# Kernel optimization log

Hardware: AMD Instinct MI355X
Metric: run time of the kernel (lower is better)

## Reference

```python
import jax, jax.numpy as jnp
import numpy as np
from jax import lax

B = 512
ITER = 3  # routing iterations


def squash(x):
    # matches torch: sn/(1+sn) * x / (sqrt(sn)+1e-6), norm over last dim
    sn = jnp.sum(x * x, axis=-1, keepdims=True)
    return sn / (1.0 + sn) * x / (jnp.sqrt(sn) + 1e-6)


def conv2d(x, w, b, stride):
    y = lax.conv_general_dilated(
        x, w, window_strides=(stride, stride), padding='VALID',
        dimension_numbers=('NCHW', 'OIHW', 'NCHW'))
    return y + b[None, :, None, None]


def setup_inputs() -> dict:
    key = jax.random.key(0)
    ks = jax.random.split(key, 6)
    x = jax.random.normal(ks[0], (B, 3, 28, 28), dtype=jnp.float32)
    conv1_w = jax.random.normal(ks[1], (256, 3, 9, 9), dtype=jnp.float32) * 0.05
    conv1_b = jnp.zeros((256,), dtype=jnp.float32)
    conv2_w = jax.random.normal(ks[2], (256, 256, 9, 9), dtype=jnp.float32) * 0.02
    conv2_b = jnp.zeros((256,), dtype=jnp.float32)
    # DigitCapsule W: (1, 32, 6, 6, 10, 8, 16) in torch; drop leading 1 here
    W = jax.random.normal(ks[3], (32, 6, 6, 10, 8, 16), dtype=jnp.float32)
    return {'x': x, 'conv1_w': conv1_w, 'conv1_b': conv1_b,
            'conv2_w': conv2_w, 'conv2_b': conv2_b, 'W': W}


def reference(x, conv1_w, conv1_b, conv2_w, conv2_b, W):
    # conv1 + relu: [B,3,28,28] -> [B,256,20,20]
    h = jax.nn.relu(conv2d(x, conv1_w, conv1_b, stride=1))
    # primary capsule conv: -> [B,256,6,6]
    h = conv2d(h, conv2_w, conv2_b, stride=2)
    # torch .view(-1, 32, 6, 6, 8) on contiguous NCHW == row-major reshape
    u = squash(jnp.reshape(h, (h.shape[0], 32, 6, 6, 8)))  # [B,32,6,6,8]
    # u_hat[b,i,j,k,o,e] = sum_d u[b,i,j,k,d] * W[i,j,k,o,d,e]
    u_hat = jnp.einsum('bijkd,ijkode->bijkoe', u, W)  # [B,32,6,6,10,16]
    b_logits = jnp.zeros(u_hat.shape[:-1], dtype=u_hat.dtype)  # [B,32,6,6,10]
    v = None
    for it in range(ITER):
        c = jax.nn.softmax(b_logits, axis=-1)
        s = jnp.sum(c[..., None] * u_hat, axis=(1, 2, 3))  # [B,10,16]
        v = squash(s)
        if it < ITER - 1:
            b_logits = b_logits + jnp.sum(
                u_hat * v[:, None, None, None], axis=-1)
    return v
```

## Files before the change

### kernel.cpp

```cpp
#include <hip/hip_runtime.h>
#include <math.h>

typedef short short8v __attribute__((ext_vector_type(8)));
typedef float float4v __attribute__((ext_vector_type(4)));

#define OFF_U     ((size_t)0)
#define OFF_A     ((size_t)18874368)
#define OFF_W1T   ((size_t)29491200)
#define OFF_WT    ((size_t)30670848)
#define OFF_SPART ((size_t)33619968)
#define OFF_VSUM  ((size_t)38862848)

__device__ inline short f2bf(float f) {
  union { float f; unsigned u; } v; v.f = f;
  unsigned r = v.u + 0x7FFFu + ((v.u >> 16) & 1u);
  return (short)(r >> 16);
}
__device__ inline float bf2f(short s) {
  union { unsigned u; float f; } v; v.u = ((unsigned)(unsigned short)s) << 16;
  return v.f;
}

__global__ __launch_bounds__(256) void prep_kernel(
    const float* __restrict__ w2, short* __restrict__ w2b,
    const float* __restrict__ w1, short* __restrict__ w1t,
    const float* __restrict__ W, short* __restrict__ Wtb) {
  __shared__ short tl[81][66];
  int bx = blockIdx.x, t = threadIdx.x;
  if (bx < 1024) {
    int co = bx >> 2, ci0 = (bx & 3) * 64;
    for (int f = t; f < 64 * 81; f += 256) {
      int cip = f / 81, tap = f % 81;
      tl[tap][cip] = f2bf(w2[((size_t)co * 256 + ci0 + cip) * 81 + tap]);
    }
    __syncthreads();
    for (int f = t; f < 81 * 64; f += 256) {
      int tap = f >> 6, cip = f & 63;
      w2b[((size_t)tap * 256 + co) * 256 + ci0 + cip] = tl[tap][cip];
    }
  } else if (bx < 1280) {
    int co = bx - 1024;
    w1t[co * 256 + t] = (t < 243) ? f2bf(w1[(size_t)co * 243 + t]) : (short)0;
  } else {
    int idx = (bx - 1280) * 256 + t;
    if (idx < 1152 * 1280) {
      int n = idx / 1280, r = idx - n * 1280;
      int o = r >> 7, de = r & 127;
      int d = de >> 4, e = de & 15;
      Wtb[(((size_t)n * 10 + o) * 16 + e) * 8 + d] = f2bf(W[idx]);
    }
  }
}

__global__ __launch_bounds__(256, 2) void conv_fused_kernel(
    const float* __restrict__ x, const short* __restrict__ w1t,
    const float* __restrict__ b1v, const short* __restrict__ w2b,
    const float* __restrict__ b2v, float* __restrict__ h2) {
  __shared__ short xsb[4704];
  __shared__ short h1l[800][40];

  int b0 = blockIdx.x * 2;
  int coh = blockIdx.y;
  int t = threadIdx.x;
  int lane = t & 63;
  int wv = t >> 6;
  int l15 = lane & 15, lq = lane >> 4;

  for (int i = t; i < 4704; i += 256) xsb[i] = f2bf(x[(size_t)b0 * 2352 + i]);

  float4v acc2[5][2];
#pragma unroll
  for (int mt = 0; mt < 5; mt++)
#pragma unroll
    for (int nt = 0; nt < 2; nt++) acc2[mt][nt] = (float4v){0.f, 0.f, 0.f, 0.f};

  int rowb[5];
#pragma unroll
  for (int mt = 0; mt < 5; mt++) {
    int m = mt * 16 + l15;
    int ab = (m >= 40) ? 1 : 0;
    int s = m - 40 * ab;
    if (s >= 36) s = 0;
    int sx = (s * 43) >> 8;
    int sy = s - 6 * sx;
    rowb[mt] = ab * 400 + sx * 40 + sy * 2;
  }
  int co[2];
#pragma unroll
  for (int nt = 0; nt < 2; nt++) co[nt] = coh * 128 + wv * 32 + nt * 16 + l15;

  int nmt = (wv == 0) ? 7 : 6;
  int px1[7], py1[7];
#pragma unroll
  for (int j = 0; j < 7; j++) {
    int pos = (wv + 4 * j) * 16 + l15;
    if (pos >= 400) pos = 0;
    px1[j] = (pos * 3277) >> 16;
    py1[j] = pos - 20 * px1[j];
  }

  for (int ch = 0; ch < 8; ch++) {
    int ci0 = ch * 32;
    __syncthreads();

    for (int bb = 0; bb < 2; bb++) {
      const short* xb = &xsb[bb * 2352];
      float4v acc1[7][2];
#pragma unroll
      for (int j = 0; j < 7; j++)
#pragma unroll
        for (int nt = 0; nt < 2; nt++) acc1[j][nt] = (float4v){0.f, 0.f, 0.f, 0.f};
#pragma unroll 1
      for (int kk = 0; kk < 8; kk++) {
        int k0 = kk * 32 + lq * 8;
        int cin = (k0 * 810) >> 16;
        int rem = k0 - 81 * cin;
        int kx = (rem * 57) >> 9;
        int ky = rem - 9 * kx;
        int nv = 243 - k0; if (nv > 8) nv = 8; if (nv < 0) nv = 0;
        int n1 = 9 - ky; if (n1 > 8) n1 = 8;
        int d2 = (kx < 8) ? (28 - ky) : (560 - ky);
        short8v b1f[2];
#pragma unroll
        for (int nt = 0; nt < 2; nt++)
          b1f[nt] = *(const short8v*)(w1t + (size_t)(ci0 + nt * 16 + l15) * 256 + k0);
#pragma unroll
        for (int j = 0; j < 7; j++) {
          if (j < nmt) {
            int o1 = cin * 784 + (px1[j] + kx) * 28 + py1[j] + ky;
            short8v a;
#pragma unroll
            for (int jj = 0; jj < 8; jj++) {
              int idx = (jj < n1) ? (o1 + jj) : (o1 + d2 + jj - n1);
              if (jj >= nv) idx = 0;
              short vsh = xb[idx];
              a[jj] = (jj < nv) ? vsh : (short)0;
            }
#pragma unroll
            for (int nt = 0; nt < 2; nt++)
              acc1[j][nt] = __builtin_amdgcn_mfma_f32_16x16x32_bf16(
                  a, b1f[nt], acc1[j][nt], 0, 0, 0);
          }
        }
      }
      float bs[2];
#pragma unroll
      for (int nt = 0; nt < 2; nt++) bs[nt] = b1v[ci0 + nt * 16 + l15];
#pragma unroll
      for (int j = 0; j < 7; j++) {
        if (j < nmt) {
#pragma unroll
          for (int nt = 0; nt < 2; nt++) {
#pragma unroll
            for (int r = 0; r < 4; r++) {
              int pos = (wv + 4 * j) * 16 + lq * 4 + r;
              float h = acc1[j][nt][r] + bs[nt];
              h1l[bb * 400 + pos][nt * 16 + l15] = f2bf(h > 0.f ? h : 0.f);
            }
          }
        }
      }
    }
    __syncthreads();

    short8v bA[2], bB[2], bC[2];
#pragma unroll
    for (int nt = 0; nt < 2; nt++) {
      const short* wb = w2b + (size_t)co[nt] * 256 + ci0 + lq * 8;
      bA[nt] = *(const short8v*)(wb);
      bB[nt] = *(const short8v*)(wb + 65536);
      bC[nt] = *(const short8v*)(wb + 2 * 65536);
    }
#pragma unroll 1
    for (int tg = 0; tg < 27; tg++) {
#pragma unroll
      for (int sl = 0; sl < 3; sl++) {
        int tap = tg * 3 + sl;
        int kx = (tap * 57) >> 9;
        int ky = tap - 9 * kx;
        int tf = tap + 3; if (tf > 80) tf = 80;
        short8v bcur[2];
#pragma unroll
        for (int nt = 0; nt < 2; nt++)
          bcur[nt] = (sl == 0) ? bA[nt] : (sl == 1) ? bB[nt] : bC[nt];
#pragma unroll
        for (int nt = 0; nt < 2; nt++) {
          short8v bn = *(const short8v*)(w2b + (size_t)tf * 65536 +
                                         (size_t)co[nt] * 256 + ci0 + lq * 8);
          if (sl == 0) bA[nt] = bn; else if (sl == 1) bB[nt] = bn; else bC[nt] = bn;
        }
        int dly = kx * 20 + ky;
#pragma unroll
        for (int mt = 0; mt < 5; mt++) {
          short8v af = *(const short8v*)&h1l[rowb[mt] + dly][lq * 8];
#pragma unroll
          for (int nt = 0; nt < 2; nt++)
            acc2[mt][nt] = __builtin_amdgcn_mfma_f32_16x16x32_bf16(
                af, bcur[nt], acc2[mt][nt], 0, 0, 0);
        }
      }
    }
  }

#pragma unroll
  for (int nt = 0; nt < 2; nt++) {
    float bias = b2v[co[nt]];
#pragma unroll
    for (int mt = 0; mt < 5; mt++) {
#pragma unroll
      for (int r = 0; r < 4; r++) {
        int m = mt * 16 + lq * 4 + r;
        int ab = (m >= 40) ? 1 : 0;
        int s = m - 40 * ab;
        if (s < 36)
          h2[((size_t)(b0 + ab) * 256 + co[nt]) * 36 + s] = acc2[mt][nt][r] + bias;
      }
    }
  }
}

__global__ __launch_bounds__(256) void s_part_kernel(
    const float* __restrict__ h2u, const short* __restrict__ Wtb,
    const float* __restrict__ vsum, float* __restrict__ spart) {
  int bt = blockIdx.x, nc = blockIdx.y;
  int t = threadIdx.x;
  int bq = t >> 4, e = t & 15;
  int b = bt * 16 + bq;
  float vsp[10];
  if (vsum != nullptr) {
#pragma unroll
    for (int o = 0; o < 10; o++) vsp[o] = vsum[(size_t)b * 160 + o * 16 + e];
  }
  float acc[10];
#pragma unroll
  for (int o = 0; o < 10; o++) acc[o] = 0.f;
  int n0 = nc * 72;
#pragma unroll 2
  for (int n = n0; n < n0 + 72; n++) {
    const float4* up = (const float4*)(h2u + ((size_t)b * 1152 + n) * 8);
    float4 u0 = up[0], u1 = up[1];
    float sn = u0.x*u0.x + u0.y*u0.y + u0.z*u0.z + u0.w*u0.w +
               u1.x*u1.x + u1.y*u1.y + u1.z*u1.z + u1.w*u1.w;
    float sc = sn / (1.f + sn) / (sqrtf(sn) + 1e-6f);
    u0.x *= sc; u0.y *= sc; u0.z *= sc; u0.w *= sc;
    u1.x *= sc; u1.y *= sc; u1.z *= sc; u1.w *= sc;
    const short8v* wp = (const short8v*)(Wtb + ((size_t)n * 160 + e) * 8);
    float uh[10];
#pragma unroll
    for (int o = 0; o < 10; o++) {
      short8v w = wp[o * 16];
      uh[o] = u0.x * bf2f(w[0]) + u0.y * bf2f(w[1]) +
              u0.z * bf2f(w[2]) + u0.w * bf2f(w[3]) +
              u1.x * bf2f(w[4]) + u1.y * bf2f(w[5]) +
              u1.z * bf2f(w[6]) + u1.w * bf2f(w[7]);
    }
    if (vsum != nullptr) {
      float bl[10];
#pragma unroll
      for (int o = 0; o < 10; o++) {
        float r = uh[o] * vsp[o];
        r += __shfl_xor(r, 1);
        r += __shfl_xor(r, 2);
        r += __shfl_xor(r, 4);
        r += __shfl_xor(r, 8);
        bl[o] = r;
      }
      float m = bl[0];
#pragma unroll
      for (int o = 1; o < 10; o++) m = fmaxf(m, bl[o]);
      float sum = 0.f;
#pragma unroll
      for (int o = 0; o < 10; o++) { bl[o] = __expf(bl[o] - m); sum += bl[o]; }
      float inv = 1.f / sum;
#pragma unroll
      for (int o = 0; o < 10; o++) acc[o] = fmaf(bl[o] * inv, uh[o], acc[o]);
    } else {
#pragma unroll
      for (int o = 0; o < 10; o++) acc[o] += uh[o];
    }
  }
  float* sp = spart + (size_t)nc * 81920 + (size_t)b * 160 + e;
#pragma unroll
  for (int o = 0; o < 10; o++) sp[o * 16] = acc[o];
}

__global__ void squash_v_kernel(const float* __restrict__ spart,
                                float* __restrict__ dst, float prescale,
                                int accumulate) {
  int g = blockIdx.x * 256 + threadIdx.x;
  if (g >= 5120) return;
  float r[16];
#pragma unroll
  for (int e = 0; e < 16; e++) r[e] = 0.f;
#pragma unroll
  for (int p = 0; p < 16; p++) {
    const float4* sp = (const float4*)(spart + (size_t)p * 81920 + (size_t)g * 16);
#pragma unroll
    for (int q = 0; q < 4; q++) {
      float4 f4 = sp[q];
      r[4 * q] += f4.x; r[4 * q + 1] += f4.y; r[4 * q + 2] += f4.z; r[4 * q + 3] += f4.w;
    }
  }
  float sn = 0.f;
#pragma unroll
  for (int e = 0; e < 16; e++) { r[e] *= prescale; sn += r[e] * r[e]; }
  float scale = sn / (1.f + sn) / (sqrtf(sn) + 1e-6f);
  float* q = dst + (size_t)g * 16;
#pragma unroll
  for (int e = 0; e < 16; e++) {
    float val = r[e] * scale;
    q[e] = accumulate ? (q[e] + val) : val;
  }
}

extern "C" void kernel_launch(void* const* d_in, const int* in_sizes, int n_in,
                              void* d_out, int out_size, void* d_ws, size_t ws_size,
                              hipStream_t stream) {
  const float* x   = (const float*)d_in[0];
  const float* w1  = (const float*)d_in[1];
  const float* b1v = (const float*)d_in[2];
  const float* w2  = (const float*)d_in[3];
  const float* b2v = (const float*)d_in[4];
  const float* W   = (const float*)d_in[5];
  float* out = (float*)d_out;

  char* ws = (char*)d_ws;
  float* u     = (float*)(ws + OFF_U);
  short* w2b   = (short*)(ws + OFF_A);
  short* w1t   = (short*)(ws + OFF_W1T);
  short* Wtb   = (short*)(ws + OFF_WT);
  float* spart = (float*)(ws + OFF_SPART);
  float* vsum  = (float*)(ws + OFF_VSUM);

  prep_kernel<<<7040, 256, 0, stream>>>(w2, w2b, w1, w1t, W, Wtb);
  conv_fused_kernel<<<dim3(256, 2), 256, 0, stream>>>(x, w1t, b1v, w2b, b2v, u);

  s_part_kernel<<<dim3(32, 16), 256, 0, stream>>>(u, Wtb, nullptr, spart);
  squash_v_kernel<<<20, 256, 0, stream>>>(spart, vsum, 0.1f, 0);
  s_part_kernel<<<dim3(32, 16), 256, 0, stream>>>(u, Wtb, vsum, spart);
  squash_v_kernel<<<20, 256, 0, stream>>>(spart, vsum, 1.0f, 1);
  s_part_kernel<<<dim3(32, 16), 256, 0, stream>>>(u, Wtb, vsum, spart);
  squash_v_kernel<<<20, 256, 0, stream>>>(spart, out, 1.0f, 0);
}
```

Baseline: 868.0 us.

## Pad conv1 K-dimension per kernel row and use shifted LDS copies for aligned loads

The conv1 weight layout is repadded so each kernel row (kx) holds 16 ky slots, zeros beyond 9. The input image is stored twice in LDS, once shifted by one element, so each 8-element A fragment becomes four aligned 32-bit loads instead of eight scalar gathers with boundary logic. This raises the conv1 K loop from 8 to 14 iterations, so more MFMAs run on padded zeros, in exchange for much cheaper operand fetch. The h1 LDS row stride also shrinks from 40 to 36 shorts, so A fragments are read as two 8-byte loads, which changes the bank mapping and LDS footprint.

New measurement: 856.9 us. Within noise of the previous version (-1.3%).

```diff
diff --git a/kernel.cpp b/kernel.cpp
--- a/kernel.cpp
+++ b/kernel.cpp
@@ -1,8 +1,10 @@
 #include <hip/hip_runtime.h>
 #include <math.h>
 
+typedef short short4v __attribute__((ext_vector_type(4)));
 typedef short short8v __attribute__((ext_vector_type(8)));
 typedef float float4v __attribute__((ext_vector_type(4)));
+typedef unsigned uint4v __attribute__((ext_vector_type(4)));
 
 #define OFF_U     ((size_t)0)
 #define OFF_A     ((size_t)18874368)
@@ -40,7 +42,15 @@
     }
   } else if (bx < 1280) {
     int co = bx - 1024;
-    w1t[co * 256 + t] = (t < 243) ? f2bf(w1[(size_t)co * 243 + t]) : (short)0;
+    for (int kp = t; kp < 448; kp += 256) {
+      short v = 0;
+      if (kp < 432) {
+        int cin = kp / 144, r = kp - cin * 144;
+        int kx = r >> 4, ky = r & 15;
+        if (ky < 9) v = f2bf(w1[(size_t)co * 243 + cin * 81 + kx * 9 + ky]);
+      }
+      w1t[co * 448 + kp] = v;
+    }
   } else {
     int idx = (bx - 1280) * 256 + t;
     if (idx < 1152 * 1280) {
@@ -56,8 +66,8 @@
     const float* __restrict__ x, const short* __restrict__ w1t,
     const float* __restrict__ b1v, const short* __restrict__ w2b,
     const float* __restrict__ b2v, float* __restrict__ h2) {
-  __shared__ short xsb[4704];
-  __shared__ short h1l[800][40];
+  __shared__ short xs2[2][2][2360];
+  __shared__ short h1l[800][36];
 
   int b0 = blockIdx.x * 2;
   int coh = blockIdx.y;
@@ -66,7 +76,17 @@
   int wv = t >> 6;
   int l15 = lane & 15, lq = lane >> 4;
 
-  for (int i = t; i < 4704; i += 256) xsb[i] = f2bf(x[(size_t)b0 * 2352 + i]);
+  if (t < 64) {
+    int c = t & 1, bb2 = (t >> 1) & 1, k = t >> 2;
+    int idx = 2351 + k;
+    if (idx < 2360 && (c == 1 || idx >= 2352)) xs2[c][bb2][idx] = 0;
+  }
+  for (int i = t; i < 4704; i += 256) {
+    int bb = i / 2352, j = i - bb * 2352;
+    short v = f2bf(x[(size_t)b0 * 2352 + i]);
+    xs2[0][bb][j] = v;
+    if (j >= 1) xs2[1][bb][j - 1] = v;
+  }
 
   float4v acc2[5][2];
 #pragma unroll
@@ -104,38 +124,31 @@
     __syncthreads();
 
     for (int bb = 0; bb < 2; bb++) {
-      const short* xb = &xsb[bb * 2352];
       float4v acc1[7][2];
 #pragma unroll
       for (int j = 0; j < 7; j++)
 #pragma unroll
         for (int nt = 0; nt < 2; nt++) acc1[j][nt] = (float4v){0.f, 0.f, 0.f, 0.f};
 #pragma unroll 1
-      for (int kk = 0; kk < 8; kk++) {
+      for (int kk = 0; kk < 14; kk++) {
         int k0 = kk * 32 + lq * 8;
-        int cin = (k0 * 810) >> 16;
-        int rem = k0 - 81 * cin;
-        int kx = (rem * 57) >> 9;
-        int ky = rem - 9 * kx;
-        int nv = 243 - k0; if (nv > 8) nv = 8; if (nv < 0) nv = 0;
-        int n1 = 9 - ky; if (n1 > 8) n1 = 8;
-        int d2 = (kx < 8) ? (28 - ky) : (560 - ky);
+        int cin = (k0 >= 288) ? 2 : ((k0 >= 144) ? 1 : 0);
+        int r = k0 - cin * 144;
+        int kx = r >> 4;
+        int kyb = r & 15;
         short8v b1f[2];
 #pragma unroll
         for (int nt = 0; nt < 2; nt++)
-          b1f[nt] = *(const short8v*)(w1t + (size_t)(ci0 + nt * 16 + l15) * 256 + k0);
+          b1f[nt] = *(const short8v*)(w1t + (size_t)(ci0 + nt * 16 + l15) * 448 + k0);
 #pragma unroll
         for (int j = 0; j < 7; j++) {
           if (j < nmt) {
-            int o1 = cin * 784 + (px1[j] + kx) * 28 + py1[j] + ky;
-            short8v a;
-#pragma unroll
-            for (int jj = 0; jj < 8; jj++) {
-              int idx = (jj < n1) ? (o1 + jj) : (o1 + d2 + jj - n1);
-              if (jj >= nv) idx = 0;
-              short vsh = xb[idx];
-              a[jj] = (jj < nv) ? vsh : (short)0;
-            }
+            int o1 = cin * 784 + (px1[j] + kx) * 28 + py1[j] + kyb;
+            if (k0 >= 432) o1 = 0;
+            int p = o1 & 1;
+            const unsigned* q = (const unsigned*)&xs2[p][bb][o1 - p];
+            uint4v w4 = {q[0], q[1], q[2], q[3]};
+            short8v a = __builtin_bit_cast(short8v, w4);
 #pragma unroll
             for (int nt = 0; nt < 2; nt++)
               acc1[j][nt] = __builtin_amdgcn_mfma_f32_16x16x32_bf16(
@@ -192,7 +205,8 @@
         int dly = kx * 20 + ky;
 #pragma unroll
         for (int mt = 0; mt < 5; mt++) {
-          short8v af = *(const short8v*)&h1l[rowb[mt] + dly][lq * 8];
+          const short4v* ap = (const short4v*)&h1l[rowb[mt] + dly][lq * 8];
+          short8v af = __builtin_shufflevector(ap[0], ap[1], 0, 1, 2, 3, 4, 5, 6, 7);
 #pragma unroll
           for (int nt = 0; nt < 2; nt++)
             acc2[mt][nt] = __builtin_amdgcn_mfma_f32_16x16x32_bf16(
```
